# Kernel tuning notes

Hardware: AMD Instinct MI355X
Metric: run time of the kernel (lower is better)

The kernel has to match this reference:

```python
import jax, jax.numpy as jnp
import numpy as np


def dwconv3x3(x, w, b):
    # depthwise 3x3, stride 1, padding 1 (SAME); x: [B,C,H,W], w: [C,1,3,3], b: [C]
    y = jax.lax.conv_general_dilated(
        x, w, window_strides=(1, 1), padding='SAME',
        dimension_numbers=('NCHW', 'OIHW', 'NCHW'),
        feature_group_count=x.shape[1])
    return y + b[None, :, None, None]


def setup_inputs() -> dict:
    B, C, K, H, W = 16, 512, 128, 64, 64
    key = jax.random.key(0)
    ks = jax.random.split(key, 8)
    return {
        'x_q': jax.random.normal(ks[0], (B, C, H, W), jnp.float32),
        'x_kv': jax.random.normal(ks[1], (B, K, H, W), jnp.float32),
        'wq': jax.random.normal(ks[2], (C, 1, 3, 3), jnp.float32) * 0.1,
        'bq': jax.random.normal(ks[3], (C,), jnp.float32) * 0.1,
        'wk': jax.random.normal(ks[4], (K, 1, 3, 3), jnp.float32) * 0.1,
        'bk': jax.random.normal(ks[5], (K,), jnp.float32) * 0.1,
        'wv': jax.random.normal(ks[6], (K, 1, 3, 3), jnp.float32) * 0.1,
        'bv': jax.random.normal(ks[7], (K,), jnp.float32) * 0.1,
    }


def reference(x_q, x_kv, wq, bq, wk, bk, wv, bv):
    q = dwconv3x3(x_q, wq, bq)          # [B,C,H,W]
    k = dwconv3x3(x_kv, wk, bk)         # [B,K,H,W]
    v = dwconv3x3(x_kv, wv, bv)         # [B,K,H,W]
    B, C, H, W = q.shape
    Kp = k.shape[1]
    qf = q.reshape(B, C, H * W)         # [B,C,N]
    kf = k.reshape(B, Kp, H * W)        # [B,K,N]
    vf = v.reshape(B, Kp, H * W)        # [B,K,N]
    # attn_weights: [B,C,K], scaled by sqrt(num_prompt)
    aw = jnp.einsum('bcn,bkn->bck', qf, kf) / (Kp ** 0.5)
    aw = jax.nn.softmax(aw, axis=-1)
    n_keep = int(0.1 * C)               # static
    aw_t = jnp.swapaxes(aw, 1, 2)       # [B,K,C]
    _, idx = jax.lax.top_k(aw_t, n_keep)  # idx: [B,K,n_keep]
    bi = jnp.arange(B)[:, None, None]
    ki = jnp.arange(Kp)[None, :, None]
    mask_t = jnp.zeros_like(aw_t).at[bi, ki, idx].set(1.0)
    aw = aw * jnp.swapaxes(mask_t, 1, 2)  # [B,C,K]
    attn_out = jnp.einsum('bck,bkn->bcn', aw, vf).reshape(B, C, H, W)
    return (x_q + attn_out, aw)
```

## Files before the change

### kernel.cpp

```cpp
#include <hip/hip_runtime.h>

#define B_ 16
#define C_ 512
#define K_ 128
#define N_ 4096
#define NKEEP 51
#define NSPLIT 8

__global__ void conv_kv_kernel(const float* __restrict__ xkv,
                               const float* __restrict__ wk, const float* __restrict__ bk,
                               const float* __restrict__ wv, const float* __restrict__ bv,
                               float* __restrict__ kb, float* __restrict__ vb) {
    int idx = blockIdx.x * 256 + threadIdx.x;
    int x = idx & 63;
    int y = (idx >> 6) & 63;
    int k = (idx >> 12) & 127;
    int b = idx >> 19;
    const float* wkp = wk + k * 9;
    const float* wvp = wv + k * 9;
    const float* xp  = xkv + (size_t)(b * K_ + k) * N_;
    float ak = bk[k], av = bv[k];
#pragma unroll
    for (int dy = 0; dy < 3; ++dy) {
        int yy = y + dy - 1;
        if (yy < 0 || yy > 63) continue;
#pragma unroll
        for (int dx = 0; dx < 3; ++dx) {
            int xx = x + dx - 1;
            if (xx < 0 || xx > 63) continue;
            float xv = xp[yy * 64 + xx];
            ak += xv * wkp[dy * 3 + dx];
            av += xv * wvp[dy * 3 + dx];
        }
    }
    kb[idx] = ak;
    vb[idx] = av;
}

__global__ __launch_bounds__(256) void qk2_kernel(const float* __restrict__ xq,
                                                  const float* __restrict__ wq,
                                                  const float* __restrict__ bq,
                                                  const float* __restrict__ kb,
                                                  float* __restrict__ part) {
    __shared__ float qs[64][64];
    __shared__ float ks[64][128];
    int blk = blockIdx.x;
    int ct  = blk & 7;
    int ns  = (blk >> 3) & 7;
    int b   = blk >> 6;
    int c0  = ct * 64;
    int r0  = ns * 8;
    int tid = threadIdx.x;

    int c_l = tid >> 2;
    int xs  = (tid & 3) << 4;
    int k_l = tid >> 1;
    int nh  = (tid & 1) << 5;
    int cg4 = (tid & 15) * 4;
    int kg8 = (tid >> 4) * 8;

    const float* wp = wq + (size_t)(c0 + c_l) * 9;
    float w00=wp[0],w01=wp[1],w02=wp[2],w10=wp[3],w11=wp[4],w12=wp[5],w20=wp[6],w21=wp[7],w22=wp[8];
    float bias = bq[c0 + c_l];
    const float* xqp = xq + ((size_t)(b * C_) + c0 + c_l) * N_;
    const float* kbp = kb + ((size_t)(b * K_) + k_l) * N_;

    float acc[4][8];
#pragma unroll
    for (int i = 0; i < 4; ++i)
#pragma unroll
        for (int j = 0; j < 8; ++j) acc[i][j] = 0.f;

    for (int rr = 0; rr < 8; ++rr) {
        int r = r0 + rr;
        __syncthreads();
        {
            const float4* src = (const float4*)(kbp + r * 64 + nh);
#pragma unroll
            for (int m = 0; m < 8; ++m) {
                float4 v = src[m];
                int nn = nh + m * 4;
                ks[nn][k_l] = v.x; ks[nn + 1][k_l] = v.y;
                ks[nn + 2][k_l] = v.z; ks[nn + 3][k_l] = v.w;
            }
        }
        {
            float a16[16];
#pragma unroll
            for (int i = 0; i < 16; ++i) a16[i] = bias;
#pragma unroll
            for (int dy = 0; dy < 3; ++dy) {
                int yy = r + dy - 1;
                if (yy < 0 || yy > 63) continue;
                const float* row = xqp + yy * 64;
                float wa = (dy == 0) ? w00 : (dy == 1) ? w10 : w20;
                float wb = (dy == 0) ? w01 : (dy == 1) ? w11 : w21;
                float wc = (dy == 0) ? w02 : (dy == 1) ? w12 : w22;
                float p = (xs == 0) ? 0.f : row[xs - 1];
                float c = row[xs];
#pragma unroll
                for (int i = 0; i < 16; ++i) {
                    int x = xs + i;
                    float n = (x == 63) ? 0.f : row[x + 1];
                    a16[i] += p * wa + c * wb + n * wc;
                    p = c; c = n;
                }
            }
#pragma unroll
            for (int i = 0; i < 16; ++i) qs[xs + i][c_l] = a16[i];
        }
        __syncthreads();
#pragma unroll 4
        for (int nn = 0; nn < 64; ++nn) {
            float4 q4  = *(const float4*)&qs[nn][cg4];
            float4 k4a = *(const float4*)&ks[nn][kg8];
            float4 k4b = *(const float4*)&ks[nn][kg8 + 4];
            float qa[4] = {q4.x, q4.y, q4.z, q4.w};
            float kk[8] = {k4a.x, k4a.y, k4a.z, k4a.w, k4b.x, k4b.y, k4b.z, k4b.w};
#pragma unroll
            for (int i = 0; i < 4; ++i)
#pragma unroll
                for (int j = 0; j < 8; ++j) acc[i][j] += qa[i] * kk[j];
        }
    }
    float* dst = part + (((size_t)ns * B_ + b) * C_ + c0 + cg4) * K_ + kg8;
#pragma unroll
    for (int i = 0; i < 4; ++i) {
        *(float4*)(dst + (size_t)i * K_)     = make_float4(acc[i][0], acc[i][1], acc[i][2], acc[i][3]);
        *(float4*)(dst + (size_t)i * K_ + 4) = make_float4(acc[i][4], acc[i][5], acc[i][6], acc[i][7]);
    }
}

__global__ void softmax_kernel(const float* __restrict__ part, float* __restrict__ aw) {
    int tid  = threadIdx.x;
    int wave = tid >> 6;
    int lane = tid & 63;
    int row  = blockIdx.x * 4 + wave;
    float v0 = 0.f, v1 = 0.f;
#pragma unroll
    for (int ns = 0; ns < NSPLIT; ++ns) {
        const float* p = part + ((size_t)ns * B_ * C_ + row) * K_;
        v0 += p[lane];
        v1 += p[lane + 64];
    }
    const float scale = 0.08838834764831845f;
    v0 *= scale; v1 *= scale;
    float m = fmaxf(v0, v1);
#pragma unroll
    for (int s = 32; s >= 1; s >>= 1) m = fmaxf(m, __shfl_xor(m, s, 64));
    float e0 = __expf(v0 - m), e1 = __expf(v1 - m);
    float s = e0 + e1;
#pragma unroll
    for (int t = 32; t >= 1; t >>= 1) s += __shfl_xor(s, t, 64);
    float inv = 1.0f / s;
    float* q = aw + (size_t)row * K_;
    q[lane] = e0 * inv;
    q[lane + 64] = e1 * inv;
}

__global__ void topk_mask_kernel(float* __restrict__ aw) {
    int tid  = threadIdx.x;
    int wave = tid >> 6, lane = tid & 63;
    int col  = blockIdx.x * 4 + wave;
    int b = col >> 7, k = col & 127;
    float* base = aw + (size_t)(b * C_) * K_ + k;
    unsigned u[8];
#pragma unroll
    for (int j = 0; j < 8; ++j)
        u[j] = __float_as_uint(base[(size_t)(j * 64 + lane) * K_]);
    unsigned T = 0;
#pragma unroll
    for (int bit = 31; bit >= 0; --bit) {
        unsigned cand = T | (1u << bit);
        int cnt = 0;
#pragma unroll
        for (int j = 0; j < 8; ++j) cnt += (u[j] >= cand) ? 1 : 0;
#pragma unroll
        for (int s = 32; s >= 1; s >>= 1) cnt += __shfl_xor(cnt, s, 64);
        if (cnt >= NKEEP) T = cand;
    }
#pragma unroll
    for (int j = 0; j < 8; ++j)
        if (u[j] < T) base[(size_t)(j * 64 + lane) * K_] = 0.0f;
}

__global__ __launch_bounds__(256) void av_kernel(const float* __restrict__ aw,
                                                 const float* __restrict__ vb,
                                                 const float* __restrict__ xq,
                                                 float* __restrict__ out) {
    __shared__ float vs[16][260];
    __shared__ float aws[16][36];
    int blk  = blockIdx.x;
    int b    = blk >> 8;
    int rest = blk & 255;
    int c0 = (rest >> 4) * 32;
    int n0 = (rest & 15) * 256;
    int tid = threadIdx.x;
    int cg = tid >> 5;
    int ng = tid & 31;
    int k_l = tid >> 4;
    int nn0 = (tid & 15) * 16;

    float acc[4][8];
#pragma unroll
    for (int i = 0; i < 4; ++i)
#pragma unroll
        for (int j = 0; j < 8; ++j) acc[i][j] = 0.f;

    for (int kc = 0; kc < K_; kc += 16) {
        __syncthreads();
        {
            const float4* src = (const float4*)(vb + (size_t)(b * K_ + kc + k_l) * N_ + n0 + nn0);
            float4* dst = (float4*)&vs[k_l][nn0];
#pragma unroll
            for (int m = 0; m < 4; ++m) dst[m] = src[m];
        }
        {
            int i0 = tid * 2;
#pragma unroll
            for (int t2 = 0; t2 < 2; ++t2) {
                int i = i0 + t2;
                int cc = i >> 4;
                int kk = i & 15;
                aws[kk][cc] = aw[(size_t)(b * C_ + c0 + cc) * K_ + kc + kk];
            }
        }
        __syncthreads();
#pragma unroll
        for (int kk = 0; kk < 16; ++kk) {
            float4 a4  = *(const float4*)&aws[kk][cg * 4];
            float4 v4a = *(const float4*)&vs[kk][ng * 8];
            float4 v4b = *(const float4*)&vs[kk][ng * 8 + 4];
            float aa[4] = {a4.x, a4.y, a4.z, a4.w};
            float av[8] = {v4a.x, v4a.y, v4a.z, v4a.w, v4b.x, v4b.y, v4b.z, v4b.w};
#pragma unroll
            for (int i = 0; i < 4; ++i)
#pragma unroll
                for (int j = 0; j < 8; ++j) acc[i][j] += aa[i] * av[j];
        }
    }
#pragma unroll
    for (int i = 0; i < 4; ++i) {
        int c = c0 + cg * 4 + i;
        size_t base = (size_t)(b * C_ + c) * N_ + n0 + ng * 8;
        const float4* xp4 = (const float4*)(xq + base);
        float4* op4 = (float4*)(out + base);
        float4 x0 = xp4[0], x1 = xp4[1];
        float4 o0, o1;
        o0.x = x0.x + acc[i][0]; o0.y = x0.y + acc[i][1];
        o0.z = x0.z + acc[i][2]; o0.w = x0.w + acc[i][3];
        o1.x = x1.x + acc[i][4]; o1.y = x1.y + acc[i][5];
        o1.z = x1.z + acc[i][6]; o1.w = x1.w + acc[i][7];
        op4[0] = o0; op4[1] = o1;
    }
}

extern "C" void kernel_launch(void* const* d_in, const int* in_sizes, int n_in,
                              void* d_out, int out_size, void* d_ws, size_t ws_size,
                              hipStream_t stream) {
    const float* xq  = (const float*)d_in[0];
    const float* xkv = (const float*)d_in[1];
    const float* wq  = (const float*)d_in[2];
    const float* bq  = (const float*)d_in[3];
    const float* wk  = (const float*)d_in[4];
    const float* bk  = (const float*)d_in[5];
    const float* wv  = (const float*)d_in[6];
    const float* bv  = (const float*)d_in[7];

    float* out0 = (float*)d_out;
    float* aw   = out0 + (size_t)B_ * C_ * N_;

    float* kb = (float*)d_ws;
    float* vb = kb + (size_t)B_ * K_ * N_;
    float* part = out0;

    conv_kv_kernel<<<(B_ * K_ * N_) / 256, 256, 0, stream>>>(xkv, wk, bk, wv, bv, kb, vb);
    qk2_kernel<<<B_ * 64, 256, 0, stream>>>(xq, wq, bq, kb, part);
    softmax_kernel<<<(B_ * C_) / 4, 256, 0, stream>>>(part, aw);
    topk_mask_kernel<<<(B_ * K_) / 4, 256, 0, stream>>>(aw);
    av_kernel<<<B_ * 256, 256, 0, stream>>>(aw, vb, xq, out0);
}
```

Baseline: 563.9 us.

## Prefetch next tile into registers in qk and av kernels, remap qk block order

In both the QK and AV GEMM kernels, the global loads for the next row or K-chunk are issued into registers right after the barrier, so they overlap with the current tile's FMA loop (register double-buffering). The QK depthwise conv now reads its input with float4 vector loads plus halo scalars instead of scalar loads. QK block indices are permuted so that consecutive blocks fall on different batches and tiles, and launch bounds request three blocks per CU. The change trades extra registers for hiding global memory latency, which may reduce occupancy or cause spills.

```diff
diff --git a/kernel.cpp b/kernel.cpp
--- a/kernel.cpp
+++ b/kernel.cpp
@@ -37,14 +37,16 @@
     vb[idx] = av;
 }
 
-__global__ __launch_bounds__(256) void qk2_kernel(const float* __restrict__ xq,
-                                                  const float* __restrict__ wq,
-                                                  const float* __restrict__ bq,
-                                                  const float* __restrict__ kb,
-                                                  float* __restrict__ part) {
+__global__ __launch_bounds__(256, 3) void qk3_kernel(const float* __restrict__ xq,
+                                                     const float* __restrict__ wq,
+                                                     const float* __restrict__ bq,
+                                                     const float* __restrict__ kb,
+                                                     float* __restrict__ part) {
     __shared__ float qs[64][64];
     __shared__ float ks[64][128];
-    int blk = blockIdx.x;
+
+    int bid = blockIdx.x;
+    int blk = (bid & 7) * 128 + (bid >> 3);
     int ct  = blk & 7;
     int ns  = (blk >> 3) & 7;
     int b   = blk >> 6;
@@ -63,7 +65,34 @@
     float w00=wp[0],w01=wp[1],w02=wp[2],w10=wp[3],w11=wp[4],w12=wp[5],w20=wp[6],w21=wp[7],w22=wp[8];
     float bias = bq[c0 + c_l];
     const float* xqp = xq + ((size_t)(b * C_) + c0 + c_l) * N_;
-    const float* kbp = kb + ((size_t)(b * K_) + k_l) * N_;
+    const float* kbp = kb + ((size_t)(b * K_) + k_l) * N_ + nh;
+
+    float4 kv[8];
+    float4 xm[3][4];
+    float  xl[3], xr[3];
+
+#define LOADROW(r)                                                             \
+    {                                                                          \
+        const float4* src = (const float4*)(kbp + (r) * 64);                   \
+        _Pragma("unroll")                                                      \
+        for (int m = 0; m < 8; ++m) kv[m] = src[m];                            \
+        _Pragma("unroll")                                                      \
+        for (int dy = 0; dy < 3; ++dy) {                                       \
+            int yy = (r) + dy - 1;                                             \
+            if (yy < 0 || yy > 63) {                                           \
+                _Pragma("unroll")                                              \
+                for (int m = 0; m < 4; ++m) xm[dy][m] = make_float4(0,0,0,0);  \
+                xl[dy] = 0.f; xr[dy] = 0.f;                                    \
+            } else {                                                           \
+                const float* row = xqp + yy * 64 + xs;                         \
+                const float4* r4 = (const float4*)row;                         \
+                _Pragma("unroll")                                              \
+                for (int m = 0; m < 4; ++m) xm[dy][m] = r4[m];                 \
+                xl[dy] = (xs == 0)  ? 0.f : row[-1];                           \
+                xr[dy] = (xs == 48) ? 0.f : row[16];                           \
+            }                                                                  \
+        }                                                                      \
+    }
 
     float acc[4][8];
 #pragma unroll
@@ -71,18 +100,15 @@
 #pragma unroll
         for (int j = 0; j < 8; ++j) acc[i][j] = 0.f;
 
+    LOADROW(r0);
+
     for (int rr = 0; rr < 8; ++rr) {
-        int r = r0 + rr;
         __syncthreads();
-        {
-            const float4* src = (const float4*)(kbp + r * 64 + nh);
-#pragma unroll
-            for (int m = 0; m < 8; ++m) {
-                float4 v = src[m];
-                int nn = nh + m * 4;
-                ks[nn][k_l] = v.x; ks[nn + 1][k_l] = v.y;
-                ks[nn + 2][k_l] = v.z; ks[nn + 3][k_l] = v.w;
-            }
+#pragma unroll
+        for (int m = 0; m < 8; ++m) {
+            int nn = nh + m * 4;
+            ks[nn][k_l]     = kv[m].x; ks[nn + 1][k_l] = kv[m].y;
+            ks[nn + 2][k_l] = kv[m].z; ks[nn + 3][k_l] = kv[m].w;
         }
         {
             float a16[16];
@@ -90,26 +116,28 @@
             for (int i = 0; i < 16; ++i) a16[i] = bias;
 #pragma unroll
             for (int dy = 0; dy < 3; ++dy) {
-                int yy = r + dy - 1;
-                if (yy < 0 || yy > 63) continue;
-                const float* row = xqp + yy * 64;
                 float wa = (dy == 0) ? w00 : (dy == 1) ? w10 : w20;
                 float wb = (dy == 0) ? w01 : (dy == 1) ? w11 : w21;
                 float wc = (dy == 0) ? w02 : (dy == 1) ? w12 : w22;
-                float p = (xs == 0) ? 0.f : row[xs - 1];
-                float c = row[xs];
-#pragma unroll
-                for (int i = 0; i < 16; ++i) {
-                    int x = xs + i;
-                    float n = (x == 63) ? 0.f : row[x + 1];
-                    a16[i] += p * wa + c * wb + n * wc;
-                    p = c; c = n;
+                float xrow[18];
+                xrow[0] = xl[dy];
+#pragma unroll
+                for (int m = 0; m < 4; ++m) {
+                    xrow[1 + 4*m]     = xm[dy][m].x;
+                    xrow[1 + 4*m + 1] = xm[dy][m].y;
+                    xrow[1 + 4*m + 2] = xm[dy][m].z;
+                    xrow[1 + 4*m + 3] = xm[dy][m].w;
                 }
+                xrow[17] = xr[dy];
+#pragma unroll
+                for (int i = 0; i < 16; ++i)
+                    a16[i] += xrow[i] * wa + xrow[i + 1] * wb + xrow[i + 2] * wc;
             }
 #pragma unroll
             for (int i = 0; i < 16; ++i) qs[xs + i][c_l] = a16[i];
         }
         __syncthreads();
+        if (rr < 7) LOADROW(r0 + rr + 1);
 #pragma unroll 4
         for (int nn = 0; nn < 64; ++nn) {
             float4 q4  = *(const float4*)&qs[nn][cg4];
@@ -123,6 +151,8 @@
                 for (int j = 0; j < 8; ++j) acc[i][j] += qa[i] * kk[j];
         }
     }
+#undef LOADROW
+
     float* dst = part + (((size_t)ns * B_ + b) * C_ + c0 + cg4) * K_ + kg8;
 #pragma unroll
     for (int i = 0; i < 4; ++i) {
@@ -200,32 +230,41 @@
     int ng = tid & 31;
     int k_l = tid >> 4;
     int nn0 = (tid & 15) * 16;
+    int i0  = tid * 2;
+    int cc0 = i0 >> 4,       kk0 = i0 & 15;
+    int cc1 = (i0 + 1) >> 4, kk1 = (i0 + 1) & 15;
+
+    float4 vv[4];
+    float  a0, a1;
+
+#define LOADAV(kc)                                                              \
+    {                                                                           \
+        const float4* src = (const float4*)(vb + (size_t)(b * K_ + (kc) + k_l) * N_ + n0 + nn0); \
+        _Pragma("unroll")                                                       \
+        for (int m = 0; m < 4; ++m) vv[m] = src[m];                             \
+        a0 = aw[(size_t)(b * C_ + c0 + cc0) * K_ + (kc) + kk0];                 \
+        a1 = aw[(size_t)(b * C_ + c0 + cc1) * K_ + (kc) + kk1];                 \
+    }
 
     float acc[4][8];
 #pragma unroll
     for (int i = 0; i < 4; ++i)
 #pragma unroll
         for (int j = 0; j < 8; ++j) acc[i][j] = 0.f;
+
+    LOADAV(0);
 
     for (int kc = 0; kc < K_; kc += 16) {
         __syncthreads();
         {
-            const float4* src = (const float4*)(vb + (size_t)(b * K_ + kc + k_l) * N_ + n0 + nn0);
             float4* dst = (float4*)&vs[k_l][nn0];
 #pragma unroll
-            for (int m = 0; m < 4; ++m) dst[m] = src[m];
-        }
-        {
-            int i0 = tid * 2;
-#pragma unroll
-            for (int t2 = 0; t2 < 2; ++t2) {
-                int i = i0 + t2;
-                int cc = i >> 4;
-                int kk = i & 15;
-                aws[kk][cc] = aw[(size_t)(b * C_ + c0 + cc) * K_ + kc + kk];
-            }
+            for (int m = 0; m < 4; ++m) dst[m] = vv[m];
+            aws[kk0][cc0] = a0;
+            aws[kk1][cc1] = a1;
         }
         __syncthreads();
+        if (kc + 16 < K_) LOADAV(kc + 16);
 #pragma unroll
         for (int kk = 0; kk < 16; ++kk) {
             float4 a4  = *(const float4*)&aws[kk][cg * 4];
@@ -239,6 +278,8 @@
                 for (int j = 0; j < 8; ++j) acc[i][j] += aa[i] * av[j];
         }
     }
+#undef LOADAV
+
 #pragma unroll
     for (int i = 0; i < 4; ++i) {
         int c = c0 + cg * 4 + i;
@@ -275,7 +316,7 @@
     float* part = out0;
 
     conv_kv_kernel<<<(B_ * K_ * N_) / 256, 256, 0, stream>>>(xkv, wk, bk, wv, bv, kb, vb);
-    qk2_kernel<<<B_ * 64, 256, 0, stream>>>(xq, wq, bq, kb, part);
+    qk3_kernel<<<B_ * 64, 256, 0, stream>>>(xq, wq, bq, kb, part);
     softmax_kernel<<<(B_ * C_) / 4, 256, 0, stream>>>(part, aw);
     topk_mask_kernel<<<(B_ * K_) / 4, 256, 0, stream>>>(aw);
     av_kernel<<<B_ * 256, 256, 0, stream>>>(aw, vb, xq, out0);
```

After: 634.2 us. 1.12x slower.
